# Kernel tuning notes

Hardware: AMD Instinct MI355X
Metric: run time of the kernel (lower is better)

## Reference

```python
import jax, jax.numpy as jnp
import numpy as np

N = 200000
E = 3200000


def _init_linear(key, fan_in, fan_out):
    kw, kb = jax.random.split(key)
    bound = 1.0 / np.sqrt(fan_in)
    W = jax.random.uniform(kw, (fan_in, fan_out), jnp.float32, -bound, bound)
    b = jax.random.uniform(kb, (fan_out,), jnp.float32, -bound, bound)
    return W, b


def setup_inputs() -> dict:
    key = jax.random.key(0)
    ks = jax.random.split(key, 8)
    latent_features = jax.random.normal(ks[0], (N, 256), jnp.float32)
    history = jax.random.uniform(ks[1], (N,), jnp.float32)
    is_subgoal = jax.random.uniform(ks[2], (N,), jnp.float32)
    edge_index = jax.random.randint(ks[3], (2, E), 0, N, dtype=jnp.int64)
    W1, b1 = _init_linear(ks[4], 258, 128)
    W2, b2 = _init_linear(ks[5], 128, 64)
    W3, b3 = _init_linear(ks[6], 64, 8)
    Wc, bc = _init_linear(ks[7], 8, 3)
    return {"latent_features": latent_features, "history": history,
            "is_subgoal": is_subgoal, "edge_index": edge_index,
            "W1": W1, "b1": b1, "W2": W2, "b2": b2,
            "W3": W3, "b3": b3, "Wc": Wc, "bc": bc}


def _gcn_conv(h, W, b, src, dst, norm, n):
    # PyG GCNConv: linear transform, then symmetric-normalized scatter-add.
    h = h @ W                                  # [n, F_out]
    msg = norm[:, None] * h[src]               # gather + edge-norm, [E+n, F_out]
    out = jax.ops.segment_sum(msg, dst, num_segments=n)
    return out + b


def reference(latent_features, history, is_subgoal, edge_index,
              W1, b1, W2, b2, W3, b3, Wc, bc):
    n = latent_features.shape[0]
    # add self-loops (GCNConv default add_self_loops=True)
    loop = jnp.arange(n, dtype=edge_index.dtype)
    src = jnp.concatenate([edge_index[0], loop])
    dst = jnp.concatenate([edge_index[1], loop])
    # symmetric normalization: deg over destination (incl. self-loops)
    deg = jax.ops.segment_sum(jnp.ones_like(dst, dtype=jnp.float32), dst,
                              num_segments=n)
    dinv = jnp.where(deg > 0, jax.lax.rsqrt(deg), 0.0)
    norm = dinv[src] * dinv[dst]               # [E+n]

    h = jnp.concatenate([latent_features, history[:, None],
                         is_subgoal[:, None]], axis=1)  # [n, 258]
    h = jax.nn.relu(_gcn_conv(h, W1, b1, src, dst, norm, n))
    h = jax.nn.relu(_gcn_conv(h, W2, b2, src, dst, norm, n))
    h = jax.nn.relu(_gcn_conv(h, W3, b3, src, dst, norm, n))
    return h @ Wc + bc                          # [n, 3]
```

## Files before the change

kernel.cpp:

```cpp
#include <hip/hip_runtime.h>
#include <hip/hip_fp16.h>


#define N_NODES 200000
#define N_EDGES 3200000
#define NBUCK 782
#define BCAP 5120

static_assert(N_NODES % 64 == 0, "tiling");
static_assert((NBUCK - 1) * 256 < N_NODES && NBUCK * 256 >= N_NODES, "buckets");

typedef unsigned int u32;
typedef _Float16 f16;
typedef __attribute__((ext_vector_type(8))) _Float16 f16x8;
typedef __attribute__((ext_vector_type(4))) _Float16 f16x4;
typedef __attribute__((ext_vector_type(4))) float f32x4;
typedef __attribute__((ext_vector_type(2))) float f32x2;


__global__ __launch_bounds__(256) void k_scatter(const int* __restrict__ src,
                                                 const int* __restrict__ dst,
                                                 int* __restrict__ bcur,
                                                 u32* __restrict__ entries) {
    __shared__ int lh[NBUCK];
    __shared__ int base[NBUCK];
    __shared__ int lcur[NBUCK];
    int t = threadIdx.x;
    for (int b = t; b < NBUCK; b += 256) lh[b] = 0;
    __syncthreads();
    long e0 = (long)blockIdx.x * 8192;
    for (int k = 0; k < 32; ++k) {
        long e = e0 + k * 256 + t;
        if (e < N_EDGES) atomicAdd(&lh[dst[e] >> 8], 1);
    }
    __syncthreads();
    for (int b = t; b < NBUCK; b += 256) {
        base[b] = lh[b] ? atomicAdd(&bcur[b], lh[b]) : 0;
        lcur[b] = 0;
    }
    __syncthreads();
    for (int k = 0; k < 32; ++k) {
        long e = e0 + k * 256 + t;
        if (e < N_EDGES) {
            int d = dst[e];
            int bkt = d >> 8;
            int p = base[bkt] + atomicAdd(&lcur[bkt], 1);
            p = p < BCAP ? p : BCAP - 1;
            entries[(size_t)bkt * BCAP + p] = ((u32)src[e] << 8) | (u32)(d & 255);
        }
    }
}


__global__ __launch_bounds__(256) void k_prep(const u32* __restrict__ entries,
                                              const int* __restrict__ bcur,
                                              int* __restrict__ rs,
                                              int* __restrict__ re,
                                              float* __restrict__ dinv,
                                              int* __restrict__ col) {
    __shared__ int lh[256];
    __shared__ int sc[256];
    __shared__ int cur[256];
    const int b = blockIdx.x, t = threadIdx.x;
    int cnt = bcur[b];
    cnt = cnt < BCAP ? cnt : BCAP;
    const u32* ent = entries + (size_t)b * BCAP;
    lh[t] = 0;
    __syncthreads();
    for (int i = t; i < cnt; i += 256) atomicAdd(&lh[ent[i] & 255], 1);
    __syncthreads();
    int my = lh[t];
    sc[t] = my;
    __syncthreads();
    for (int o = 1; o < 256; o <<= 1) {
        int v = (t >= o) ? sc[t - o] : 0;
        __syncthreads();
        sc[t] += v;
        __syncthreads();
    }
    int excl = sc[t] - my;
    int node = b * 256 + t;
    if (node < N_NODES) {
        rs[node] = b * BCAP + excl;
        re[node] = b * BCAP + excl + my;
        dinv[node] = rsqrtf((float)(my + 1));
    }
    cur[t] = b * BCAP + excl;
    __syncthreads();
    for (int i = t; i < cnt; i += 256) {
        u32 en = ent[i];
        int p = atomicAdd(&cur[en & 255], 1);
        col[p] = (int)(en >> 8);
    }
}


__global__ __launch_bounds__(256) void k_prepw(const float* __restrict__ W,
                                               f16* __restrict__ Wth,
                                               f16* __restrict__ Wtl) {
    int t = blockIdx.x * 256 + threadIdx.x;
    int k = t >> 7;
    int f = t & 127;
    float w = W[k * 128 + f];
    f16 hi = (f16)w;
    f16 lo = (f16)(w - (float)hi);
    Wth[f * 256 + k] = hi;
    Wtl[f * 256 + k] = lo;
}


__global__ __launch_bounds__(256) void k_prepw2(const float* __restrict__ W2,
                                                f16* __restrict__ Wh,
                                                f16* __restrict__ Wl) {
    int t = blockIdx.x * 256 + threadIdx.x;
    int k = t >> 6;
    int f = t & 63;
    float w = W2[k * 64 + f];
    f16 hi = (f16)w;
    Wh[f * 128 + k] = hi;
    Wl[f * 128 + k] = (f16)(w - (float)hi);
}


__global__ __launch_bounds__(1024) void k_gemm1(const float* __restrict__ X,
                                                const float* __restrict__ hist,
                                                const float* __restrict__ subg,
                                                const float* __restrict__ W,
                                                const f16* __restrict__ Wth,
                                                const f16* __restrict__ Wtl,
                                                const float* __restrict__ dinv,
                                                __half2* __restrict__ g1) {
    __shared__ f16 Ws[2][128 * 256];
    const int t = threadIdx.x;

    {
        const int r = t >> 3;
        const int seg = t & 7;
        const f16* gh = Wth + r * 256 + seg * 32;
        const f16* gl = Wtl + r * 256 + seg * 32;
        const int sw = (r & 7) << 4;
        const int base = r * 512 + seg * 64;
        char* wsh = (char*)&Ws[0][0];
        char* wsl = (char*)&Ws[1][0];
#pragma unroll
        for (int q = 0; q < 4; ++q) {
            *(f16x8*)(wsh + ((base + q * 16) ^ sw)) = *(const f16x8*)(gh + q * 8);
            *(f16x8*)(wsl + ((base + q * 16) ^ sw)) = *(const f16x8*)(gl + q * 8);
        }
    }

    const int wv = t >> 6;
    const int l = t & 63;
    const int l15 = l & 15;
    const int lk = l >> 4;
    const int nb = blockIdx.x * 256;
    const int node = nb + wv * 16 + l15;
    const int xrow = node < N_NODES ? node : N_NODES - 1;
    const float* xbase = X + (size_t)xrow * 256 + lk * 8;

    f32x4 acc[8];
#pragma unroll
    for (int fb = 0; fb < 8; ++fb) acc[fb] = (f32x4){0.f, 0.f, 0.f, 0.f};

    float4 pa = *(const float4*)(xbase + 0);
    float4 pb = *(const float4*)(xbase + 4);

    __syncthreads();

    const char* wsh = (const char*)&Ws[0][0];
    const char* wsl = (const char*)&Ws[1][0];
    const int sw = (l15 & 7) << 4;

    for (int kc = 0; kc < 256; kc += 32) {
        float xs[8] = {pa.x, pa.y, pa.z, pa.w, pb.x, pb.y, pb.z, pb.w};
        if (kc + 32 < 256) {
            pa = *(const float4*)(xbase + kc + 32);
            pb = *(const float4*)(xbase + kc + 36);
        }
        union { f16 h[8]; f16x8 v; } H, L;
#pragma unroll
        for (int i = 0; i < 8; ++i) {
            f16 h = (f16)xs[i];
            H.h[i] = h;
            L.h[i] = (f16)(xs[i] - (float)h);
        }
        f16x8 xh = H.v, xl = L.v;

        const int koff = ((kc + lk * 8) * 2) ^ sw;
#pragma unroll
        for (int fb = 0; fb < 8; ++fb) {
            const int off = (fb * 16 + l15) * 512 + koff;
            f16x8 wh = *(const f16x8*)(wsh + off);
            f16x8 wl = *(const f16x8*)(wsl + off);
            acc[fb] = __builtin_amdgcn_mfma_f32_16x16x32_f16(wh, xh, acc[fb], 0, 0, 0);
            acc[fb] = __builtin_amdgcn_mfma_f32_16x16x32_f16(wh, xl, acc[fb], 0, 0, 0);
            acc[fb] = __builtin_amdgcn_mfma_f32_16x16x32_f16(wl, xh, acc[fb], 0, 0, 0);
        }
    }

    const bool ok = node < N_NODES;
    const float hh = hist[xrow];
    const float ss = subg[xrow];
    const float dv = dinv[xrow];
    char* orow = (char*)g1 + (size_t)node * 256;
#pragma unroll
    for (int fb = 0; fb < 8; ++fb) {
        const int f0 = fb * 16 + lk * 4;
        float4 w6 = *(const float4*)(W + 256 * 128 + f0);
        float4 w7 = *(const float4*)(W + 257 * 128 + f0);
        union { f16 h[4]; float2 v; } o;
        o.h[0] = (f16)((acc[fb][0] + hh * w6.x + ss * w7.x) * dv);
        o.h[1] = (f16)((acc[fb][1] + hh * w6.y + ss * w7.y) * dv);
        o.h[2] = (f16)((acc[fb][2] + hh * w6.z + ss * w7.z) * dv);
        o.h[3] = (f16)((acc[fb][3] + hh * w6.w + ss * w7.w) * dv);
        if (ok) *(float2*)(orow + fb * 32 + lk * 8) = o.v;
    }
}


__global__ __launch_bounds__(1024) void k_ag2(const __half2* __restrict__ g,
                                              const int* __restrict__ rs,
                                              const int* __restrict__ re,
                                              const int* __restrict__ col,
                                              const float* __restrict__ dinv,
                                              const float* __restrict__ bias,
                                              const f16* __restrict__ W2hg,
                                              const f16* __restrict__ W2lg,
                                              __half2* __restrict__ g2) {
    __shared__ f16 Xh[64][136];
    __shared__ f16 Xl[64][136];
    __shared__ f16 Wh[64][136];
    __shared__ f16 Wl[64][136];
    const int t = threadIdx.x;
    const int nb = blockIdx.x * 64;

    {
        const int r = t >> 4;
        const int sg = (t & 15) * 8;
        *(f16x8*)&Wh[r][sg] = *(const f16x8*)(W2hg + r * 128 + sg);
        *(f16x8*)&Wl[r][sg] = *(const f16x8*)(W2lg + r * 128 + sg);
    }

    const int wv = t >> 6;
    const int l = t & 63;
    const int hf = l >> 5;
    const int ln = l & 31;
    const f16x4* gp = (const f16x4*)g;
    const float4 b4 = *(const float4*)(bias + ln * 4);
    const int n0 = nb + wv * 4 + hf * 2;
    const int n1 = n0 + 1;
    f32x4 a0 = (f32x4){0.f, 0.f, 0.f, 0.f};
    f32x4 a1 = (f32x4){0.f, 0.f, 0.f, 0.f};
    int i0 = rs[n0], e0i = re[n0];
    int i1 = rs[n1], e1i = re[n1];
    while (i0 + 8 <= e0i && i1 + 8 <= e1i) {
        u32 offA[8], offB[8];
        f16x4 hA[8], hB[8];
#pragma unroll
        for (int u = 0; u < 8; ++u) offA[u] = ((u32)col[i0 + u] << 5) + ln;
#pragma unroll
        for (int u = 0; u < 8; ++u) offB[u] = ((u32)col[i1 + u] << 5) + ln;
#pragma unroll
        for (int u = 0; u < 8; ++u) hA[u] = gp[offA[u]];
#pragma unroll
        for (int u = 0; u < 8; ++u) hB[u] = gp[offB[u]];
#pragma unroll
        for (int u = 0; u < 8; ++u) a0 += __builtin_convertvector(hA[u], f32x4);
#pragma unroll
        for (int u = 0; u < 8; ++u) a1 += __builtin_convertvector(hB[u], f32x4);
        i0 += 8;
        i1 += 8;
    }
    for (; i0 + 8 <= e0i; i0 += 8) {
        u32 off[8];
        f16x4 h[8];
#pragma unroll
        for (int u = 0; u < 8; ++u) off[u] = ((u32)col[i0 + u] << 5) + ln;
#pragma unroll
        for (int u = 0; u < 8; ++u) h[u] = gp[off[u]];
#pragma unroll
        for (int u = 0; u < 8; ++u) a0 += __builtin_convertvector(h[u], f32x4);
    }
    for (; i1 + 8 <= e1i; i1 += 8) {
        u32 off[8];
        f16x4 h[8];
#pragma unroll
        for (int u = 0; u < 8; ++u) off[u] = ((u32)col[i1 + u] << 5) + ln;
#pragma unroll
        for (int u = 0; u < 8; ++u) h[u] = gp[off[u]];
#pragma unroll
        for (int u = 0; u < 8; ++u) a1 += __builtin_convertvector(h[u], f32x4);
    }
    for (; i0 < e0i; ++i0) a0 += __builtin_convertvector(gp[((u32)col[i0] << 5) + ln], f32x4);
    for (; i1 < e1i; ++i1) a1 += __builtin_convertvector(gp[((u32)col[i1] << 5) + ln], f32x4);

#pragma unroll
    for (int i = 0; i < 2; ++i) {
        const int node = i ? n1 : n0;
        f32x4 a = i ? a1 : a0;
        f32x4 fs = __builtin_convertvector(gp[((u32)node << 5) + ln], f32x4);
        const float di = dinv[node];
        float v0 = fmaxf(di * (a[0] + fs[0]) + b4.x, 0.f);
        float v1 = fmaxf(di * (a[1] + fs[1]) + b4.y, 0.f);
        float v2 = fmaxf(di * (a[2] + fs[2]) + b4.z, 0.f);
        float v3 = fmaxf(di * (a[3] + fs[3]) + b4.w, 0.f);
        f16 h0 = (f16)v0, h1 = (f16)v1, h2 = (f16)v2, h3 = (f16)v3;
        f16x4 hi = {h0, h1, h2, h3};
        f16x4 lo = {(f16)(v0 - (float)h0), (f16)(v1 - (float)h1),
                    (f16)(v2 - (float)h2), (f16)(v3 - (float)h3)};
        *(f16x4*)&Xh[node - nb][ln * 4] = hi;
        *(f16x4*)&Xl[node - nb][ln * 4] = lo;
    }
    __syncthreads();

    const int l15 = l & 15;
    const int lk = l >> 4;
    const int nw = wv & 3;
    const int fw = wv >> 2;
    f32x4 acc = (f32x4){0.f, 0.f, 0.f, 0.f};
#pragma unroll
    for (int kc = 0; kc < 128; kc += 32) {
        f16x8 xh = *(const f16x8*)&Xh[nw * 16 + l15][kc + lk * 8];
        f16x8 xl = *(const f16x8*)&Xl[nw * 16 + l15][kc + lk * 8];
        f16x8 wh = *(const f16x8*)&Wh[fw * 16 + l15][kc + lk * 8];
        f16x8 wl = *(const f16x8*)&Wl[fw * 16 + l15][kc + lk * 8];
        acc = __builtin_amdgcn_mfma_f32_16x16x32_f16(wh, xh, acc, 0, 0, 0);
        acc = __builtin_amdgcn_mfma_f32_16x16x32_f16(wh, xl, acc, 0, 0, 0);
        acc = __builtin_amdgcn_mfma_f32_16x16x32_f16(wl, xh, acc, 0, 0, 0);
    }
    const int node = nb + nw * 16 + l15;
    const float dv = dinv[node];
    union { f16 h[4]; float2 v; } o;
#pragma unroll
    for (int r = 0; r < 4; ++r) o.h[r] = (f16)(acc[r] * dv);
    *(float2*)((char*)g2 + (size_t)node * 128 + fw * 32 + lk * 8) = o.v;
}


__global__ __launch_bounds__(256) void k_ag3(const __half2* __restrict__ g,
                                             const int* __restrict__ rs,
                                             const int* __restrict__ re,
                                             const int* __restrict__ col,
                                             const float* __restrict__ dinv,
                                             const float* __restrict__ bias,
                                             const float* __restrict__ W3,
                                             float* __restrict__ g3) {
    __shared__ float h3s[32][68];
    __shared__ float W3t[8][68];
    const int t = threadIdx.x;
    const int nb = blockIdx.x * 32;

    for (int i = t; i < 512; i += 256) {
        int k = i & 63, f = i >> 6;
        W3t[f][k] = W3[k * 8 + f];
    }

    const int wv = t >> 6;
    const int l = t & 63;
    const int q = l >> 4;
    const int ln = l & 15;
    const f16x4* gp = (const f16x4*)g;
    const float4 b4 = *(const float4*)(bias + ln * 4);
    const int n0 = nb + wv * 8 + q * 2;
    const int n1 = n0 + 1;
    f32x4 a0 = (f32x4){0.f, 0.f, 0.f, 0.f};
    f32x4 a1 = (f32x4){0.f, 0.f, 0.f, 0.f};
    int i0 = rs[n0], e0i = re[n0];
    int i1 = rs[n1], e1i = re[n1];
    while (i0 + 8 <= e0i && i1 + 8 <= e1i) {
        u32 offA[8], offB[8];
        f16x4 hA[8], hB[8];
#pragma unroll
        for (int u = 0; u < 8; ++u) offA[u] = ((u32)col[i0 + u] << 4) + ln;
#pragma unroll
        for (int u = 0; u < 8; ++u) offB[u] = ((u32)col[i1 + u] << 4) + ln;
#pragma unroll
        for (int u = 0; u < 8; ++u) hA[u] = gp[offA[u]];
#pragma unroll
        for (int u = 0; u < 8; ++u) hB[u] = gp[offB[u]];
#pragma unroll
        for (int u = 0; u < 8; ++u) a0 += __builtin_convertvector(hA[u], f32x4);
#pragma unroll
        for (int u = 0; u < 8; ++u) a1 += __builtin_convertvector(hB[u], f32x4);
        i0 += 8;
        i1 += 8;
    }
    for (; i0 + 8 <= e0i; i0 += 8) {
        u32 off[8];
        f16x4 h[8];
#pragma unroll
        for (int u = 0; u < 8; ++u) off[u] = ((u32)col[i0 + u] << 4) + ln;
#pragma unroll
        for (int u = 0; u < 8; ++u) h[u] = gp[off[u]];
#pragma unroll
        for (int u = 0; u < 8; ++u) a0 += __builtin_convertvector(h[u], f32x4);
    }
    for (; i1 + 8 <= e1i; i1 += 8) {
        u32 off[8];
        f16x4 h[8];
#pragma unroll
        for (int u = 0; u < 8; ++u) off[u] = ((u32)col[i1 + u] << 4) + ln;
#pragma unroll
        for (int u = 0; u < 8; ++u) h[u] = gp[off[u]];
#pragma unroll
        for (int u = 0; u < 8; ++u) a1 += __builtin_convertvector(h[u], f32x4);
    }
    for (; i0 < e0i; ++i0) a0 += __builtin_convertvector(gp[((u32)col[i0] << 4) + ln], f32x4);
    for (; i1 < e1i; ++i1) a1 += __builtin_convertvector(gp[((u32)col[i1] << 4) + ln], f32x4);

#pragma unroll
    for (int i = 0; i < 2; ++i) {
        const int node = i ? n1 : n0;
        f32x4 a = i ? a1 : a0;
        f32x4 fs = __builtin_convertvector(gp[((u32)node << 4) + ln], f32x4);
        const float di = dinv[node];
        float4 o;
        o.x = fmaxf(di * (a[0] + fs[0]) + b4.x, 0.f);
        o.y = fmaxf(di * (a[1] + fs[1]) + b4.y, 0.f);
        o.z = fmaxf(di * (a[2] + fs[2]) + b4.z, 0.f);
        o.w = fmaxf(di * (a[3] + fs[3]) + b4.w, 0.f);
        *(float4*)&h3s[node - nb][ln * 4] = o;
    }
    __syncthreads();

    const int node = t >> 3;
    const int f = t & 7;
    float acc = 0.f;
#pragma unroll
    for (int k4 = 0; k4 < 16; ++k4) {
        float4 x = *(const float4*)&h3s[node][k4 * 4];
        float4 w = *(const float4*)&W3t[f][k4 * 4];
        acc += x.x * w.x + x.y * w.y + x.z * w.z + x.w * w.w;
    }
    g3[(size_t)(nb + node) * 8 + f] = dinv[nb + node] * acc;
}


__global__ __launch_bounds__(256) void k_agf(const float* __restrict__ g,
                                             const int* __restrict__ rs,
                                             const int* __restrict__ re,
                                             const int* __restrict__ col,
                                             const float* __restrict__ dinv,
                                             const float* __restrict__ bias,
                                             const float* __restrict__ Wc,
                                             const float* __restrict__ bc,
                                             float* __restrict__ out) {
    __shared__ float h4s[64][10];
    __shared__ float Wcs[24];
    __shared__ float bcs[3];
    const int t = threadIdx.x;
    const int nb = blockIdx.x * 64;
    if (t < 24) Wcs[t] = Wc[t];
    if (t < 3) bcs[t] = bc[t];

    const int node = t >> 2;
    const int c = t & 3;
    const f32x2* gp = (const f32x2*)g;
    const float2 b2 = *(const float2*)(bias + c * 2);
    f32x2 a = (f32x2){0.f, 0.f};
    const int s = rs[nb + node];
    const int e = re[nb + node];
    int idx = s;
    for (; idx + 16 <= e; idx += 16) {
        u32 off[16];
        f32x2 v[16];
#pragma unroll
        for (int u = 0; u < 16; ++u) off[u] = ((u32)col[idx + u] << 2) + c;
#pragma unroll
        for (int u = 0; u < 16; ++u) v[u] = gp[off[u]];
#pragma unroll
        for (int u = 0; u < 16; ++u) a += v[u];
    }
    for (; idx + 8 <= e; idx += 8) {
        u32 off[8];
        f32x2 v[8];
#pragma unroll
        for (int u = 0; u < 8; ++u) off[u] = ((u32)col[idx + u] << 2) + c;
#pragma unroll
        for (int u = 0; u < 8; ++u) v[u] = gp[off[u]];
#pragma unroll
        for (int u = 0; u < 8; ++u) a += v[u];
    }
    for (; idx < e; ++idx) a += gp[((u32)col[idx] << 2) + c];
    a += gp[((u32)(nb + node) << 2) + c];
    const float di = dinv[nb + node];
    float2 o;
    o.x = fmaxf(di * a[0] + b2.x, 0.f);
    o.y = fmaxf(di * a[1] + b2.y, 0.f);
    *(float2*)&h4s[node][c * 2] = o;
    __syncthreads();

    if ((t & 3) < 3) {
        const int n2 = t >> 2;
        const int cc = t & 3;
        float o2 = bcs[cc];
#pragma unroll
        for (int k = 0; k < 8; ++k) o2 += h4s[n2][k] * Wcs[k * 3 + cc];
        out[(size_t)(nb + n2) * 3 + cc] = o2;
    }
}


extern "C" void kernel_launch(void* const* d_in, const int* in_sizes, int n_in,
                              void* d_out, int out_size, void* d_ws, size_t ws_size,
                              hipStream_t stream) {
    const float* latent = (const float*)d_in[0];
    const float* hist = (const float*)d_in[1];
    const float* subg = (const float*)d_in[2];
    const int* eidx = (const int*)d_in[3];
    const float* W1 = (const float*)d_in[4];
    const float* b1 = (const float*)d_in[5];
    const float* W2 = (const float*)d_in[6];
    const float* b2 = (const float*)d_in[7];
    const float* W3 = (const float*)d_in[8];
    const float* b3 = (const float*)d_in[9];
    const float* Wc = (const float*)d_in[10];
    const float* bc = (const float*)d_in[11];
    float* outp = (float*)d_out;

    char* ws = (char*)d_ws;
    size_t off = 0;
    auto take = [&](size_t bytes) -> void* {
        void* p = ws + off;
        off += (bytes + 255) & ~(size_t)255;
        return p;
    };
    float* dinv = (float*)take((size_t)N_NODES * 4);
    int* rs = (int*)take((size_t)N_NODES * 4);
    int* re = (int*)take((size_t)N_NODES * 4);
    int* col = (int*)take((size_t)NBUCK * BCAP * 4);
    u32* entries = (u32*)take((size_t)NBUCK * BCAP * 4);
    int* bcur = (int*)take((size_t)NBUCK * 4);
    __half2* bufH = (__half2*)take((size_t)N_NODES * 128 * 2);
    __half2* bufG2 = (__half2*)take((size_t)N_NODES * 64 * 2);
    float* bufG3 = (float*)take((size_t)N_NODES * 8 * 4);
    f16* Wth = (f16*)take((size_t)128 * 256 * 2);
    f16* Wtl = (f16*)take((size_t)128 * 256 * 2);
    f16* W2h = (f16*)take((size_t)64 * 128 * 2);
    f16* W2l = (f16*)take((size_t)64 * 128 * 2);

    const int* srcp = eidx;
    const int* dstp = eidx + N_EDGES;

    const int scat_blocks = (N_EDGES + 8191) / 8192;

    hipMemsetAsync(bcur, 0, (size_t)NBUCK * 4, stream);
    k_prepw<<<128, 256, 0, stream>>>(W1, Wth, Wtl);
    k_prepw2<<<32, 256, 0, stream>>>(W2, W2h, W2l);
    k_scatter<<<scat_blocks, 256, 0, stream>>>(srcp, dstp, bcur, entries);
    k_prep<<<NBUCK, 256, 0, stream>>>(entries, bcur, rs, re, dinv, col);

    k_gemm1<<<(N_NODES + 255) / 256, 1024, 0, stream>>>(latent, hist, subg, W1, Wth, Wtl, dinv, bufH);
    k_ag2<<<N_NODES / 64, 1024, 0, stream>>>(bufH, rs, re, col, dinv, b1, W2h, W2l, bufG2);
    k_ag3<<<N_NODES / 32, 256, 0, stream>>>(bufG2, rs, re, col, dinv, b2, W3, bufG3);
    k_agf<<<N_NODES / 64, 256, 0, stream>>>(bufG3, rs, re, col, dinv, b3, Wc, bc, outp);
}
```

Measured before the change: 790.5 us.

## Sort CSR neighbor lists per node and simplify gather loops to one node at a time

After building the CSR column array, each thread insertion-sorts its node's neighbor list (up to 48 entries) so gathers walk source rows in ascending address order, aiming for better cache and TLB locality. The two aggregation kernels drop the interleaved two-node gather loop and process each node sequentially, which lowers register pressure but gives up the memory-level parallelism of keeping sixteen gathers in flight. The sort adds serial per-thread work using a local array that may spill to scratch, and it can leave lists longer than 48 only partly sorted, which changes summation order slightly.

Result: slower. 838.3 us (+6.1%).

```diff
diff --git a/kernel.cpp b/kernel.cpp
--- a/kernel.cpp
+++ b/kernel.cpp
@@ -91,6 +91,20 @@
         u32 en = ent[i];
         int p = atomicAdd(&cur[en & 255], 1);
         col[p] = (int)(en >> 8);
+    }
+    __syncthreads();
+
+    if (node < N_NODES && my > 1) {
+        const int base = b * BCAP + excl;
+        const int nbuf = my < 48 ? my : 48;
+        int buf[48];
+        for (int i = 0; i < nbuf; ++i) buf[i] = col[base + i];
+        for (int i = 1; i < nbuf; ++i) {
+            int v = buf[i], j = i - 1;
+            while (j >= 0 && buf[j] > v) { buf[j + 1] = buf[j]; --j; }
+            buf[j + 1] = v;
+        }
+        for (int i = 0; i < nbuf; ++i) col[base + i] = buf[i];
     }
 }
 
@@ -247,57 +261,24 @@
     const int ln = l & 31;
     const f16x4* gp = (const f16x4*)g;
     const float4 b4 = *(const float4*)(bias + ln * 4);
-    const int n0 = nb + wv * 4 + hf * 2;
-    const int n1 = n0 + 1;
-    f32x4 a0 = (f32x4){0.f, 0.f, 0.f, 0.f};
-    f32x4 a1 = (f32x4){0.f, 0.f, 0.f, 0.f};
-    int i0 = rs[n0], e0i = re[n0];
-    int i1 = rs[n1], e1i = re[n1];
-    while (i0 + 8 <= e0i && i1 + 8 <= e1i) {
-        u32 offA[8], offB[8];
-        f16x4 hA[8], hB[8];
-#pragma unroll
-        for (int u = 0; u < 8; ++u) offA[u] = ((u32)col[i0 + u] << 5) + ln;
-#pragma unroll
-        for (int u = 0; u < 8; ++u) offB[u] = ((u32)col[i1 + u] << 5) + ln;
-#pragma unroll
-        for (int u = 0; u < 8; ++u) hA[u] = gp[offA[u]];
-#pragma unroll
-        for (int u = 0; u < 8; ++u) hB[u] = gp[offB[u]];
-#pragma unroll
-        for (int u = 0; u < 8; ++u) a0 += __builtin_convertvector(hA[u], f32x4);
-#pragma unroll
-        for (int u = 0; u < 8; ++u) a1 += __builtin_convertvector(hB[u], f32x4);
-        i0 += 8;
-        i1 += 8;
-    }
-    for (; i0 + 8 <= e0i; i0 += 8) {
-        u32 off[8];
-        f16x4 h[8];
-#pragma unroll
-        for (int u = 0; u < 8; ++u) off[u] = ((u32)col[i0 + u] << 5) + ln;
-#pragma unroll
-        for (int u = 0; u < 8; ++u) h[u] = gp[off[u]];
-#pragma unroll
-        for (int u = 0; u < 8; ++u) a0 += __builtin_convertvector(h[u], f32x4);
-    }
-    for (; i1 + 8 <= e1i; i1 += 8) {
-        u32 off[8];
-        f16x4 h[8];
-#pragma unroll
-        for (int u = 0; u < 8; ++u) off[u] = ((u32)col[i1 + u] << 5) + ln;
-#pragma unroll
-        for (int u = 0; u < 8; ++u) h[u] = gp[off[u]];
-#pragma unroll
-        for (int u = 0; u < 8; ++u) a1 += __builtin_convertvector(h[u], f32x4);
-    }
-    for (; i0 < e0i; ++i0) a0 += __builtin_convertvector(gp[((u32)col[i0] << 5) + ln], f32x4);
-    for (; i1 < e1i; ++i1) a1 += __builtin_convertvector(gp[((u32)col[i1] << 5) + ln], f32x4);
-
-#pragma unroll
     for (int i = 0; i < 2; ++i) {
-        const int node = i ? n1 : n0;
-        f32x4 a = i ? a1 : a0;
+        const int nloc = wv * 4 + hf * 2 + i;
+        const int node = nb + nloc;
+        f32x4 a = (f32x4){0.f, 0.f, 0.f, 0.f};
+        int idx = rs[node];
+        const int e = re[node];
+        for (; idx + 8 <= e; idx += 8) {
+            u32 off[8];
+            f16x4 h[8];
+#pragma unroll
+            for (int u = 0; u < 8; ++u) off[u] = ((u32)col[idx + u] << 5) + ln;
+#pragma unroll
+            for (int u = 0; u < 8; ++u) h[u] = gp[off[u]];
+#pragma unroll
+            for (int u = 0; u < 8; ++u) a += __builtin_convertvector(h[u], f32x4);
+        }
+        for (; idx < e; ++idx)
+            a += __builtin_convertvector(gp[((u32)col[idx] << 5) + ln], f32x4);
         f32x4 fs = __builtin_convertvector(gp[((u32)node << 5) + ln], f32x4);
         const float di = dinv[node];
         float v0 = fmaxf(di * (a[0] + fs[0]) + b4.x, 0.f);
@@ -308,8 +289,8 @@
         f16x4 hi = {h0, h1, h2, h3};
         f16x4 lo = {(f16)(v0 - (float)h0), (f16)(v1 - (float)h1),
                     (f16)(v2 - (float)h2), (f16)(v3 - (float)h3)};
-        *(f16x4*)&Xh[node - nb][ln * 4] = hi;
-        *(f16x4*)&Xl[node - nb][ln * 4] = lo;
+        *(f16x4*)&Xh[nloc][ln * 4] = hi;
+        *(f16x4*)&Xl[nloc][ln * 4] = lo;
     }
     __syncthreads();
 
@@ -361,57 +342,24 @@
     const int ln = l & 15;
     const f16x4* gp = (const f16x4*)g;
     const float4 b4 = *(const float4*)(bias + ln * 4);
-    const int n0 = nb + wv * 8 + q * 2;
-    const int n1 = n0 + 1;
-    f32x4 a0 = (f32x4){0.f, 0.f, 0.f, 0.f};
-    f32x4 a1 = (f32x4){0.f, 0.f, 0.f, 0.f};
-    int i0 = rs[n0], e0i = re[n0];
-    int i1 = rs[n1], e1i = re[n1];
-    while (i0 + 8 <= e0i && i1 + 8 <= e1i) {
-        u32 offA[8], offB[8];
-        f16x4 hA[8], hB[8];
-#pragma unroll
-        for (int u = 0; u < 8; ++u) offA[u] = ((u32)col[i0 + u] << 4) + ln;
-#pragma unroll
-        for (int u = 0; u < 8; ++u) offB[u] = ((u32)col[i1 + u] << 4) + ln;
-#pragma unroll
-        for (int u = 0; u < 8; ++u) hA[u] = gp[offA[u]];
-#pragma unroll
-        for (int u = 0; u < 8; ++u) hB[u] = gp[offB[u]];
-#pragma unroll
-        for (int u = 0; u < 8; ++u) a0 += __builtin_convertvector(hA[u], f32x4);
-#pragma unroll
-        for (int u = 0; u < 8; ++u) a1 += __builtin_convertvector(hB[u], f32x4);
-        i0 += 8;
-        i1 += 8;
-    }
-    for (; i0 + 8 <= e0i; i0 += 8) {
-        u32 off[8];
-        f16x4 h[8];
-#pragma unroll
-        for (int u = 0; u < 8; ++u) off[u] = ((u32)col[i0 + u] << 4) + ln;
-#pragma unroll
-        for (int u = 0; u < 8; ++u) h[u] = gp[off[u]];
-#pragma unroll
-        for (int u = 0; u < 8; ++u) a0 += __builtin_convertvector(h[u], f32x4);
-    }
-    for (; i1 + 8 <= e1i; i1 += 8) {
-        u32 off[8];
-        f16x4 h[8];
-#pragma unroll
-        for (int u = 0; u < 8; ++u) off[u] = ((u32)col[i1 + u] << 4) + ln;
-#pragma unroll
-        for (int u = 0; u < 8; ++u) h[u] = gp[off[u]];
-#pragma unroll
-        for (int u = 0; u < 8; ++u) a1 += __builtin_convertvector(h[u], f32x4);
-    }
-    for (; i0 < e0i; ++i0) a0 += __builtin_convertvector(gp[((u32)col[i0] << 4) + ln], f32x4);
-    for (; i1 < e1i; ++i1) a1 += __builtin_convertvector(gp[((u32)col[i1] << 4) + ln], f32x4);
-
-#pragma unroll
     for (int i = 0; i < 2; ++i) {
-        const int node = i ? n1 : n0;
-        f32x4 a = i ? a1 : a0;
+        const int nloc = wv * 8 + q * 2 + i;
+        const int node = nb + nloc;
+        f32x4 a = (f32x4){0.f, 0.f, 0.f, 0.f};
+        int idx = rs[node];
+        const int e = re[node];
+        for (; idx + 8 <= e; idx += 8) {
+            u32 off[8];
+            f16x4 h[8];
+#pragma unroll
+            for (int u = 0; u < 8; ++u) off[u] = ((u32)col[idx + u] << 4) + ln;
+#pragma unroll
+            for (int u = 0; u < 8; ++u) h[u] = gp[off[u]];
+#pragma unroll
+            for (int u = 0; u < 8; ++u) a += __builtin_convertvector(h[u], f32x4);
+        }
+        for (; idx < e; ++idx)
+            a += __builtin_convertvector(gp[((u32)col[idx] << 4) + ln], f32x4);
         f32x4 fs = __builtin_convertvector(gp[((u32)node << 4) + ln], f32x4);
         const float di = dinv[node];
         float4 o;
@@ -419,7 +367,7 @@
         o.y = fmaxf(di * (a[1] + fs[1]) + b4.y, 0.f);
         o.z = fmaxf(di * (a[2] + fs[2]) + b4.z, 0.f);
         o.w = fmaxf(di * (a[3] + fs[3]) + b4.w, 0.f);
-        *(float4*)&h3s[node - nb][ln * 4] = o;
+        *(float4*)&h3s[nloc][ln * 4] = o;
     }
     __syncthreads();
 
```
